# Kernel tuning notes

Hardware: AMD Instinct MI355X
Metric: run time of the kernel (lower is better)

## Reference

```python
import jax, jax.numpy as jnp
import numpy as np
from jax import lax

B, N, NIN, NOUT, K = 8, 4096, 64, 128, 32
RATIO, R = 0.25, 0.15
M = int(N * RATIO)
DIM = NIN + 4       # x_j concat 4 point-pair features


def setup_inputs() -> dict:
    key = jax.random.key(0)
    ks = jax.random.split(key, 10)
    x = jax.random.normal(ks[0], (B, N, NIN), jnp.float32)
    pos = jax.random.uniform(ks[1], (B, N, 3), jnp.float32)
    nrm = jax.random.normal(ks[2], (B, N, 3), jnp.float32)
    norm = nrm / jnp.linalg.norm(nrm, axis=-1, keepdims=True)
    batch = jnp.broadcast_to(jnp.arange(B, dtype=jnp.int32)[:, None], (B, N))
    s = 0.05
    W1 = jax.random.normal(ks[3], (DIM, DIM), jnp.float32) * s
    b1 = jnp.zeros((DIM,), jnp.float32)
    W2 = jax.random.normal(ks[4], (DIM, DIM), jnp.float32) * s
    b2 = jnp.zeros((DIM,), jnp.float32)
    W3 = jax.random.normal(ks[5], (DIM, NOUT), jnp.float32) * s
    b3 = jnp.zeros((NOUT,), jnp.float32)
    return dict(x=x, pos=pos, norm=norm, batch=batch,
                W1=W1, b1=b1, W2=W2, b2=b2, W3=W3, b3=b3)


def fps(pos):
    """Farthest point sampling, deterministic start at index 0. pos: [N,3] -> [M] int32."""
    n = pos.shape[0]
    def step(carry, _):
        dists, last = carry
        d = jnp.sum((pos - pos[last]) ** 2, axis=-1)
        dists = jnp.minimum(dists, d)
        nxt = jnp.argmax(dists).astype(jnp.int32)
        return (dists, nxt), last
    init = (jnp.full((n,), jnp.inf, pos.dtype), jnp.int32(0))
    (_, _), idx = lax.scan(step, init, None, length=M)
    return idx


def _angle(v1, v2):
    c = jnp.cross(v1, v2)
    return jnp.arctan2(jnp.linalg.norm(c, axis=-1), jnp.sum(v1 * v2, axis=-1))


def reference(x, pos, norm, batch, W1, b1, W2, b2, W3, b3):
    # batch is implicit in the leading B dim (equal-size clouds); arg kept for parity.
    idx = jax.vmap(fps)(pos)                                   # [B,M]
    pos_s = jnp.take_along_axis(pos, idx[..., None], axis=1)   # [B,M,3]
    norm_s = jnp.take_along_axis(norm, idx[..., None], axis=1) # [B,M,3]

    # radius neighbor search: K nearest within R per sampled center
    d2 = jnp.sum((pos_s[:, :, None, :] - pos[:, None, :, :]) ** 2, axis=-1)  # [B,M,N]
    masked = jnp.where(d2 <= R * R, d2, jnp.inf)
    negv, nbr = lax.top_k(-masked, K)                          # [B,M,K]
    valid = jnp.isfinite(negv)                                 # self always valid (d2=0)

    gather = jax.vmap(lambda a, i: a[i])                       # per-batch fancy gather
    x_j = gather(x, nbr)        # [B,M,K,NIN]
    pos_j = gather(pos, nbr)    # [B,M,K,3]
    norm_j = gather(norm, nbr)  # [B,M,K,3]

    d = pos_j - pos_s[:, :, None, :]                           # pos_j - pos_i
    n_i = jnp.broadcast_to(norm_s[:, :, None, :], norm_j.shape)
    ppf = jnp.stack([
        jnp.linalg.norm(d, axis=-1),
        _angle(n_i, d),
        _angle(norm_j, d),
        _angle(n_i, norm_j),
    ], axis=-1)                                                # [B,M,K,4]

    msg = jnp.concatenate([x_j, ppf], axis=-1)                 # [B,M,K,DIM]
    h = jax.nn.relu(msg @ W1 + b1)
    h = jax.nn.relu(h @ W2 + b2)
    h = jnp.where(valid[..., None], h, -jnp.inf)
    agg = jnp.max(h, axis=2)                                   # max aggregation [B,M,DIM]
    out = jax.nn.relu(agg @ W3 + b3)                           # global_nn [B,M,NOUT]
    return out, pos_s, idx
```

## Files before the change

kernel.cpp:

```cpp
#include <hip/hip_runtime.h>
#include <hip/hip_bf16.h>
#include <math.h>

#define BB 8
#define NN 4096
#define NIN 64
#define NOUTF 128
#define KNB 32
#define MM 1024
#define DIM 68
#define CAP 320

typedef float f32x2 __attribute__((ext_vector_type(2)));

__device__ __forceinline__ f32x2 pk_add(f32x2 a, f32x2 b)
{
    f32x2 d;
    asm("v_pk_add_f32 %0, %1, %2" : "=v"(d) : "v"(a), "v"(b));
    return d;
}
__device__ __forceinline__ f32x2 pk_mul(f32x2 a, f32x2 b)
{
    f32x2 d;
    asm("v_pk_mul_f32 %0, %1, %2" : "=v"(d) : "v"(a), "v"(b));
    return d;
}

__device__ __forceinline__ f32x2 pkmax(f32x2 a, f32x2 b)
{
    f32x2 r; r.x = fmaxf(a.x, b.x); r.y = fmaxf(a.y, b.y); return r;
}

template <int CTRL>
__device__ __forceinline__ float dppmax(float v)
{
    int m = __builtin_amdgcn_update_dpp(__float_as_int(v), __float_as_int(v),
                                        CTRL, 0xF, 0xF, false);
    return fmaxf(v, __int_as_float(m));
}

__global__ __launch_bounds__(256) void fps_kernel(
    const float* __restrict__ pos,
    int* __restrict__ idx_ws,
    float* __restrict__ out_pos_s, float* __restrict__ out_idx)
{
#pragma clang fp contract(off)
    __shared__ float4 posL[NN];
    __shared__ f32x2  slot[2][4];

    const int b    = blockIdx.x;
    const int tid  = threadIdx.x;
    const int wv   = tid >> 6;
    const int lane = tid & 63;
    const float* pb = pos + (size_t)b * NN * 3;

    f32x2 X[8], Y[8], Z[8], D[8];
#pragma unroll
    for (int j = 0; j < 8; ++j) {
        int pA = tid * 16 + 2 * j;
        X[j].x = pb[pA * 3 + 0]; X[j].y = pb[pA * 3 + 3];
        Y[j].x = pb[pA * 3 + 1]; Y[j].y = pb[pA * 3 + 4];
        Z[j].x = pb[pA * 3 + 2]; Z[j].y = pb[pA * 3 + 5];
        D[j].x = INFINITY;       D[j].y = INFINITY;
    }
#pragma unroll
    for (int j = 0; j < 16; ++j) {
        int p2 = tid + 256 * j;
        posL[p2] = make_float4(pb[p2 * 3 + 0], pb[p2 * 3 + 1],
                               pb[p2 * 3 + 2], 0.0f);
    }
    __syncthreads();

    int   last = 0;
    float lx = pb[0], ly = pb[1], lz = pb[2];

#pragma unroll 2
    for (int t = 0; t < MM; ++t) {
        if (tid == 0) {
            int base = b * MM + t;
            idx_ws[base]  = last;
            out_idx[base] = (float)last;
            out_pos_s[base * 3 + 0] = lx;
            out_pos_s[base * 3 + 1] = ly;
            out_pos_s[base * 3 + 2] = lz;
        }

        float nx = -lx, ny = -ly, nz = -lz;
        f32x2 nx2; nx2.x = nx; nx2.y = nx;
        f32x2 ny2; ny2.x = ny; ny2.y = ny;
        f32x2 nz2; nz2.x = nz; nz2.y = nz;

#pragma unroll
        for (int j = 0; j < 8; ++j) {
            f32x2 dx = pk_add(X[j], nx2);
            f32x2 dy = pk_add(Y[j], ny2);
            f32x2 dz = pk_add(Z[j], nz2);
            f32x2 xx = pk_mul(dx, dx);
            f32x2 yy = pk_mul(dy, dy);
            f32x2 zz = pk_mul(dz, dz);
            f32x2 s  = pk_add(pk_add(xx, yy), zz);
            D[j].x = fminf(D[j].x, s.x);
            D[j].y = fminf(D[j].y, s.y);
        }
        f32x2 m0 = pkmax(pkmax(D[0], D[1]), pkmax(D[2], D[3]));
        f32x2 m1 = pkmax(pkmax(D[4], D[5]), pkmax(D[6], D[7]));
        f32x2 mm = pkmax(m0, m1);
        float bv = fmaxf(mm.x, mm.y);

        int k0 = (D[0].x == bv) ? 0  : ((D[0].y == bv) ? 1  : 16);
        int k1 = (D[1].x == bv) ? 2  : ((D[1].y == bv) ? 3  : 16);
        int k2 = (D[2].x == bv) ? 4  : ((D[2].y == bv) ? 5  : 16);
        int k3 = (D[3].x == bv) ? 6  : ((D[3].y == bv) ? 7  : 16);
        int k4 = (D[4].x == bv) ? 8  : ((D[4].y == bv) ? 9  : 16);
        int k5 = (D[5].x == bv) ? 10 : ((D[5].y == bv) ? 11 : 16);
        int k6 = (D[6].x == bv) ? 12 : ((D[6].y == bv) ? 13 : 16);
        int k7 = (D[7].x == bv) ? 14 : ((D[7].y == bv) ? 15 : 16);
        k0 = min(k0, k4); k1 = min(k1, k5); k2 = min(k2, k6); k3 = min(k3, k7);
        k0 = min(k0, k2); k1 = min(k1, k3);
        int kmin = min(k0, k1);
        int p_cand = tid * 16 + kmin;

        float r = bv;
        r = dppmax<0x111>(r);
        r = dppmax<0x112>(r);
        r = dppmax<0x114>(r);
        r = dppmax<0x118>(r);
        r = dppmax<0x142>(r);
        r = dppmax<0x143>(r);
        float wmax = __int_as_float(__builtin_amdgcn_readlane(__float_as_int(r), 63));

        unsigned long long msk = __ballot(bv == wmax);
        int wl = __ffsll((long long)msk) - 1;
        int pwin_wave = __builtin_amdgcn_readlane(p_cand, wl);

        const int p_ = t & 1;
        if (lane == 0) {
            f32x2 sv; sv.x = wmax; sv.y = __int_as_float(pwin_wave);
            slot[p_][wv] = sv;
        }
        __syncthreads();

        f32x2 s0 = slot[p_][0], s1 = slot[p_][1];
        f32x2 s2 = slot[p_][2], s3 = slot[p_][3];
        float cv = s0.x; int ci = __float_as_int(s0.y);
        {
            int i1 = __float_as_int(s1.y);
            bool bt = (s1.x > cv) || (s1.x == cv && i1 < ci);
            cv = bt ? s1.x : cv; ci = bt ? i1 : ci;
        }
        {
            int i2 = __float_as_int(s2.y);
            bool bt = (s2.x > cv) || (s2.x == cv && i2 < ci);
            cv = bt ? s2.x : cv; ci = bt ? i2 : ci;
        }
        {
            int i3 = __float_as_int(s3.y);
            bool bt = (s3.x > cv) || (s3.x == cv && i3 < ci);
            cv = bt ? s3.x : cv; ci = bt ? i3 : ci;
        }

        float4 cw = posL[ci];
        last = ci; lx = cw.x; ly = cw.y; lz = cw.z;
    }
}

__global__ __launch_bounds__(256) void radius_kernel(
    const float* __restrict__ pos,
    const float* __restrict__ pos_s,
    int* __restrict__ nbr_ws, int* __restrict__ nvalid_ws)
{
    __shared__ float d2L[4][CAP];
    __shared__ int   idL[4][CAP];
    __shared__ int   cntL[4];

    const int wv = threadIdx.x >> 6, lane = threadIdx.x & 63;
    const int c = blockIdx.x * 4 + wv;
    const int b = c >> 10;
    const float RSQ = 0.0225f;

    if (lane == 0) cntL[wv] = 0;

    float cx = pos_s[c * 3 + 0];
    float cy = pos_s[c * 3 + 1];
    float cz = pos_s[c * 3 + 2];
    const float* pb = pos + (size_t)b * NN * 3;

    for (int it = 0; it < NN / 64; ++it) {
        int p = it * 64 + lane;
        float dx = __fsub_rn(cx, pb[p * 3 + 0]);
        float dy = __fsub_rn(cy, pb[p * 3 + 1]);
        float dz = __fsub_rn(cz, pb[p * 3 + 2]);
        float d2 = __fadd_rn(__fadd_rn(__fmul_rn(dx, dx), __fmul_rn(dy, dy)),
                             __fmul_rn(dz, dz));
        if (d2 <= RSQ) {
            int slot = atomicAdd(&cntL[wv], 1);
            if (slot < CAP) { d2L[wv][slot] = d2; idL[wv][slot] = p; }
        }
    }
    int n = cntL[wv];
    if (n > CAP) n = CAP;

    if (n <= KNB) {
        if (lane == 0) nvalid_ws[c] = n;
        if (lane < n) nbr_ws[c * KNB + lane] = idL[wv][lane];
    } else {
        if (lane == 0) nvalid_ws[c] = KNB;
        for (int a = lane; a < n; a += 64) {
            float da = d2L[wv][a]; int ia = idL[wv][a];
            int r = 0;
            for (int jj = 0; jj < n; ++jj) {
                float dj = d2L[wv][jj]; int ij = idL[wv][jj];
                r += (dj < da || (dj == da && ij < ia)) ? 1 : 0;
            }
            if (r < KNB) nbr_ws[c * KNB + r] = ia;
        }
    }
}

__device__ __forceinline__ float angle3(float ax, float ay, float az,
                                        float bx, float by, float bz)
{
    float cx = ay * bz - az * by;
    float cy = az * bx - ax * bz;
    float cz = ax * by - ay * bx;
    float cn = sqrtf(cx * cx + cy * cy + cz * cz);
    float dt = ax * bx + ay * by + az * bz;
    return atan2f(cn, dt);
}

__device__ __forceinline__ void layer_pass(const float* __restrict__ inL,
                                           const float* __restrict__ Ws,
                                           const float* __restrict__ bs,
                                           float* __restrict__ outL, int t)
{
    const int e = t & 63, wvi = t >> 6;
    for (int jg = wvi; jg < 17; jg += 4) {
        float ax = bs[jg * 4 + 0];
        float ay = bs[jg * 4 + 1];
        float az = bs[jg * 4 + 2];
        float aw = bs[jg * 4 + 3];
#pragma unroll 4
        for (int i = 0; i < DIM; ++i) {
            float m = inL[e * 69 + i];
            const float4 w = *reinterpret_cast<const float4*>(Ws + i * DIM + jg * 4);
            ax = fmaf(m, w.x, ax);
            ay = fmaf(m, w.y, ay);
            az = fmaf(m, w.z, az);
            aw = fmaf(m, w.w, aw);
        }
        outL[e * 69 + jg * 4 + 0] = fmaxf(ax, 0.0f);
        outL[e * 69 + jg * 4 + 1] = fmaxf(ay, 0.0f);
        outL[e * 69 + jg * 4 + 2] = fmaxf(az, 0.0f);
        outL[e * 69 + jg * 4 + 3] = fmaxf(aw, 0.0f);
    }
}

__global__ __launch_bounds__(256) void mlp_kernel(
    const float* __restrict__ x, const float* __restrict__ pos,
    const float* __restrict__ norm,
    const float* __restrict__ W1, const float* __restrict__ b1,
    const float* __restrict__ W2, const float* __restrict__ b2,
    const float* __restrict__ W3, const float* __restrict__ b3,
    const int* __restrict__ idx_ws, const float* __restrict__ pos_s,
    const int* __restrict__ nbr_ws, const int* __restrict__ nvalid_ws,
    float* __restrict__ out)
{
    __shared__ alignas(16) float W1s[DIM * DIM];
    __shared__ alignas(16) float W2s[DIM * DIM];
    __shared__ float b1s[DIM], b2s[DIM];
    __shared__ float msgL[64 * 69];
    __shared__ float h1L[64 * 69];
    __shared__ float aggL[2 * DIM];
    __shared__ int   nvL[2], jLs[64];

    const int t = threadIdx.x;
    const int cg0 = blockIdx.x * 2;

    for (int u = t; u < DIM * DIM; u += 256) { W1s[u] = W1[u]; W2s[u] = W2[u]; }
    if (t < DIM) { b1s[t] = b1[t]; b2s[t] = b2[t]; }
    if (t < 2) nvL[t] = min(nvalid_ws[cg0 + t], KNB);
    __syncthreads();

    const int e = t & 63, fc = t >> 6;
    const int lc = e >> 5, slot = e & 31;
    const int c = cg0 + lc;
    const int b = c >> 10;

    if (fc == 0) {
        int nv = nvL[lc];
        jLs[e] = (slot < nv) ? nbr_ws[c * KNB + slot] : 0;
    }
    __syncthreads();

    const int j = jLs[e];
    {
        const float* xj = x + ((size_t)b * NN + j) * NIN + fc * 16;
#pragma unroll
        for (int r = 0; r < 4; ++r) {
            float4 v = *reinterpret_cast<const float4*>(xj + r * 4);
            msgL[e * 69 + fc * 16 + r * 4 + 0] = v.x;
            msgL[e * 69 + fc * 16 + r * 4 + 1] = v.y;
            msgL[e * 69 + fc * 16 + r * 4 + 2] = v.z;
            msgL[e * 69 + fc * 16 + r * 4 + 3] = v.w;
        }
    }
    if (fc == 0) {
        float pix = pos_s[c * 3 + 0];
        float piy = pos_s[c * 3 + 1];
        float piz = pos_s[c * 3 + 2];
        int ic = idx_ws[c];
        const float* pj_ = pos  + ((size_t)b * NN + j) * 3;
        const float* nj_ = norm + ((size_t)b * NN + j) * 3;
        const float* ni_ = norm + ((size_t)b * NN + ic) * 3;
        float dx = pj_[0] - pix, dy = pj_[1] - piy, dz = pj_[2] - piz;
        float nix = ni_[0], niy = ni_[1], niz = ni_[2];
        float njx = nj_[0], njy = nj_[1], njz = nj_[2];
        msgL[e * 69 + 64] = sqrtf(dx * dx + dy * dy + dz * dz);
        msgL[e * 69 + 65] = angle3(nix, niy, niz, dx, dy, dz);
        msgL[e * 69 + 66] = angle3(njx, njy, njz, dx, dy, dz);
        msgL[e * 69 + 67] = angle3(nix, niy, niz, njx, njy, njz);
    }
    __syncthreads();

    layer_pass(msgL, W1s, b1s, h1L, t);
    __syncthreads();
    layer_pass(h1L, W2s, b2s, msgL, t);
    __syncthreads();

    if (t < 2 * DIM) {
        int cc = t / DIM, jf = t % DIM;
        int nv = nvL[cc];
        float v = -INFINITY;
        for (int s = 0; s < nv; ++s)
            v = fmaxf(v, msgL[(cc * 32 + s) * 69 + jf]);
        aggL[cc * DIM + jf] = v;
    }
    __syncthreads();

    {
        int cc = t >> 7, o = t & 127;
        int cgl = cg0 + cc;
        float acc = b3[o];
#pragma unroll 4
        for (int i = 0; i < DIM; ++i)
            acc = fmaf(aggL[cc * DIM + i], W3[i * NOUTF + o], acc);
        out[(size_t)cgl * NOUTF + o] = fmaxf(acc, 0.0f);
    }
}

extern "C" void kernel_launch(void* const* d_in, const int* in_sizes, int n_in,
                              void* d_out, int out_size, void* d_ws, size_t ws_size,
                              hipStream_t stream)
{
    const float* x    = (const float*)d_in[0];
    const float* pos  = (const float*)d_in[1];
    const float* norm = (const float*)d_in[2];
    const float* W1 = (const float*)d_in[4];
    const float* b1 = (const float*)d_in[5];
    const float* W2 = (const float*)d_in[6];
    const float* b2 = (const float*)d_in[7];
    const float* W3 = (const float*)d_in[8];
    const float* b3 = (const float*)d_in[9];

    float* out       = (float*)d_out;
    float* out_pos_s = out + (size_t)BB * MM * NOUTF;
    float* out_idx   = out_pos_s + (size_t)BB * MM * 3;

    char* ws = (char*)d_ws;
    int*   idx_ws    = (int*)ws;
    int*   nbr_ws    = (int*)(ws + 131072);
    int*   nvalid_ws = (int*)(ws + 131072 + (size_t)BB * MM * KNB * 4);

    fps_kernel<<<dim3(BB), dim3(256), 0, stream>>>(pos, idx_ws,
                                                   out_pos_s, out_idx);
    radius_kernel<<<dim3((BB * MM) / 4), dim3(256), 0, stream>>>(pos, out_pos_s,
                                                                 nbr_ws, nvalid_ws);
    mlp_kernel<<<dim3((BB * MM) / 2), dim3(256), 0, stream>>>(
        x, pos, norm, W1, b1, W2, b2, W3, b3,
        idx_ws, out_pos_s, nbr_ws, nvalid_ws, out);
}
```

Measured before the change: 1.013 ms.

## Buffer FPS outputs in shared memory and register-block MLP layer columns

The FPS kernel now records each selected index and position in shared memory during the serial loop and writes them to global memory in one coalesced pass at the end. This takes the per-iteration global stores by thread 0 out of the latency-critical loop. The MLP layer pass also changes from an outer loop over column groups to holding four or five float4 accumulators per thread, so each input row element is read from LDS once per layer instead of once per column group. The cost is higher register pressure and extra shared memory in the FPS kernel.

```diff
diff --git a/kernel.cpp b/kernel.cpp
--- a/kernel.cpp
+++ b/kernel.cpp
@@ -47,6 +47,8 @@
 #pragma clang fp contract(off)
     __shared__ float4 posL[NN];
     __shared__ f32x2  slot[2][4];
+    __shared__ float4 emitP[MM];
+    __shared__ int    emitI[MM];
 
     const int b    = blockIdx.x;
     const int tid  = threadIdx.x;
@@ -77,12 +79,8 @@
 #pragma unroll 2
     for (int t = 0; t < MM; ++t) {
         if (tid == 0) {
-            int base = b * MM + t;
-            idx_ws[base]  = last;
-            out_idx[base] = (float)last;
-            out_pos_s[base * 3 + 0] = lx;
-            out_pos_s[base * 3 + 1] = ly;
-            out_pos_s[base * 3 + 2] = lz;
+            emitP[t] = make_float4(lx, ly, lz, 0.0f);
+            emitI[t] = last;
         }
 
         float nx = -lx, ny = -ly, nz = -lz;
@@ -161,6 +159,18 @@
 
         float4 cw = posL[ci];
         last = ci; lx = cw.x; ly = cw.y; lz = cw.z;
+    }
+
+    __syncthreads();
+    for (int u = tid; u < MM; u += 256) {
+        float4 rec = emitP[u];
+        int    id  = emitI[u];
+        int base = b * MM + u;
+        idx_ws[base]  = id;
+        out_idx[base] = (float)id;
+        out_pos_s[base * 3 + 0] = rec.x;
+        out_pos_s[base * 3 + 1] = rec.y;
+        out_pos_s[base * 3 + 2] = rec.z;
     }
 }
 
@@ -228,30 +238,56 @@
     return atan2f(cn, dt);
 }
 
+__device__ __forceinline__ float4 fma4(float m, float4 w, float4 a)
+{
+    a.x = fmaf(m, w.x, a.x);
+    a.y = fmaf(m, w.y, a.y);
+    a.z = fmaf(m, w.z, a.z);
+    a.w = fmaf(m, w.w, a.w);
+    return a;
+}
+
 __device__ __forceinline__ void layer_pass(const float* __restrict__ inL,
                                            const float* __restrict__ Ws,
                                            const float* __restrict__ bs,
                                            float* __restrict__ outL, int t)
 {
     const int e = t & 63, wvi = t >> 6;
-    for (int jg = wvi; jg < 17; jg += 4) {
-        float ax = bs[jg * 4 + 0];
-        float ay = bs[jg * 4 + 1];
-        float az = bs[jg * 4 + 2];
-        float aw = bs[jg * 4 + 3];
+    const bool has5 = (wvi == 0);
+    const int j0 = wvi * 4, j1 = (wvi + 4) * 4, j2 = (wvi + 8) * 4,
+              j3 = (wvi + 12) * 4, j4 = 64;
+
+    float4 a0 = *reinterpret_cast<const float4*>(bs + j0);
+    float4 a1 = *reinterpret_cast<const float4*>(bs + j1);
+    float4 a2 = *reinterpret_cast<const float4*>(bs + j2);
+    float4 a3 = *reinterpret_cast<const float4*>(bs + j3);
+    float4 a4 = has5 ? *reinterpret_cast<const float4*>(bs + j4)
+                     : make_float4(0.f, 0.f, 0.f, 0.f);
+
+    const float* row = inL + e * 69;
 #pragma unroll 4
-        for (int i = 0; i < DIM; ++i) {
-            float m = inL[e * 69 + i];
-            const float4 w = *reinterpret_cast<const float4*>(Ws + i * DIM + jg * 4);
-            ax = fmaf(m, w.x, ax);
-            ay = fmaf(m, w.y, ay);
-            az = fmaf(m, w.z, az);
-            aw = fmaf(m, w.w, aw);
-        }
-        outL[e * 69 + jg * 4 + 0] = fmaxf(ax, 0.0f);
-        outL[e * 69 + jg * 4 + 1] = fmaxf(ay, 0.0f);
-        outL[e * 69 + jg * 4 + 2] = fmaxf(az, 0.0f);
-        outL[e * 69 + jg * 4 + 3] = fmaxf(aw, 0.0f);
+    for (int i = 0; i < DIM; ++i) {
+        float m = row[i];
+        const float* wr = Ws + i * DIM;
+        a0 = fma4(m, *reinterpret_cast<const float4*>(wr + j0), a0);
+        a1 = fma4(m, *reinterpret_cast<const float4*>(wr + j1), a1);
+        a2 = fma4(m, *reinterpret_cast<const float4*>(wr + j2), a2);
+        a3 = fma4(m, *reinterpret_cast<const float4*>(wr + j3), a3);
+        if (has5) a4 = fma4(m, *reinterpret_cast<const float4*>(wr + j4), a4);
+    }
+
+    float* orow = outL + e * 69;
+    orow[j0 + 0] = fmaxf(a0.x, 0.f); orow[j0 + 1] = fmaxf(a0.y, 0.f);
+    orow[j0 + 2] = fmaxf(a0.z, 0.f); orow[j0 + 3] = fmaxf(a0.w, 0.f);
+    orow[j1 + 0] = fmaxf(a1.x, 0.f); orow[j1 + 1] = fmaxf(a1.y, 0.f);
+    orow[j1 + 2] = fmaxf(a1.z, 0.f); orow[j1 + 3] = fmaxf(a1.w, 0.f);
+    orow[j2 + 0] = fmaxf(a2.x, 0.f); orow[j2 + 1] = fmaxf(a2.y, 0.f);
+    orow[j2 + 2] = fmaxf(a2.z, 0.f); orow[j2 + 3] = fmaxf(a2.w, 0.f);
+    orow[j3 + 0] = fmaxf(a3.x, 0.f); orow[j3 + 1] = fmaxf(a3.y, 0.f);
+    orow[j3 + 2] = fmaxf(a3.z, 0.f); orow[j3 + 3] = fmaxf(a3.w, 0.f);
+    if (has5) {
+        orow[64] = fmaxf(a4.x, 0.f); orow[65] = fmaxf(a4.y, 0.f);
+        orow[66] = fmaxf(a4.z, 0.f); orow[67] = fmaxf(a4.w, 0.f);
     }
 }
 
@@ -267,7 +303,8 @@
 {
     __shared__ alignas(16) float W1s[DIM * DIM];
     __shared__ alignas(16) float W2s[DIM * DIM];
-    __shared__ float b1s[DIM], b2s[DIM];
+    __shared__ alignas(16) float b1s[DIM];
+    __shared__ alignas(16) float b2s[DIM];
     __shared__ float msgL[64 * 69];
     __shared__ float h1L[64 * 69];
     __shared__ float aggL[2 * DIM];
```

Measured after the change: 956.8 us. 5.5% less time.
